# Kernel tuning notes

Measured on AMD Instinct MI355X. Metric: run time of the kernel, lower is better.

The kernel has to match this reference:

```python
import jax, jax.numpy as jnp
import numpy as np
import math

NUM_HEADS = 16
ROPE_BASE = 10000.0


def _rotate_half(x):
    d = x.shape[-1] // 2
    return jnp.concatenate([-x[..., d:], x[..., :d]], axis=-1)


def setup_inputs() -> dict:
    key = jax.random.key(0)
    ks = jax.random.split(key, 6)
    B, S, H = 2, 2048, 2048
    x = jax.random.normal(ks[0], (B, S, H), dtype=jnp.float32)
    # xavier_uniform for square [H,H]: limit = sqrt(6/(H+H))
    lim = math.sqrt(6.0 / (H + H))
    Wq = jax.random.uniform(ks[1], (H, H), minval=-lim, maxval=lim, dtype=jnp.float32)
    Wk = jax.random.uniform(ks[2], (H, H), minval=-lim, maxval=lim, dtype=jnp.float32)
    Wv = jax.random.uniform(ks[3], (H, H), minval=-lim, maxval=lim, dtype=jnp.float32)
    Wo = jax.random.uniform(ks[4], (H, H), minval=-lim, maxval=lim, dtype=jnp.float32)
    # bias_matrix initialized as tril(randn*0.02), matching _init_weights
    bias_matrix = jnp.tril(jax.random.normal(ks[5], (S, S), dtype=jnp.float32) * 0.02)
    return {"x": x, "Wq": Wq, "Wk": Wk, "Wv": Wv, "Wo": Wo, "bias_matrix": bias_matrix}


def reference(x, Wq, Wk, Wv, Wo, bias_matrix):
    B, S, hidden = x.shape
    H = NUM_HEADS
    D = hidden // H

    # projections (torch Linear: y = x @ W.T)
    def proj(W):
        return jnp.einsum('bsh,eh->bse', x, W).reshape(B, S, H, D).transpose(0, 2, 1, 3)

    q, k, v = proj(Wq), proj(Wk), proj(Wv)  # [B,H,S,D]

    # rotary embeddings
    inv_freq = 1.0 / (ROPE_BASE ** (jnp.arange(0, D, 2, dtype=jnp.float32) / D))
    t = jnp.arange(S, dtype=jnp.float32)
    freqs = t[:, None] * inv_freq[None, :]          # [S, D/2]
    emb = jnp.concatenate([freqs, freqs], axis=-1)  # [S, D]
    cos = jnp.cos(emb)[None, None]                  # [1,1,S,D]
    sin = jnp.sin(emb)[None, None]

    q = q * cos + _rotate_half(q) * sin
    k = k * cos + _rotate_half(k) * sin

    # contextual bias: bias_matrix[:S,:S], broadcast over batch & heads
    bias = bias_matrix[:S, :S][None, None]          # [1,1,S,S]
    bmean = jnp.mean(bias, axis=-1, keepdims=True) * 0.1  # [1,1,S,1]
    q = q + bmean
    k = k + bmean

    scores = jnp.einsum('bhqd,bhkd->bhqk', q, k) / math.sqrt(D)
    scores = scores + bias

    causal = jnp.triu(jnp.ones((S, S), dtype=bool), k=1)
    scores = jnp.where(causal[None, None], -jnp.inf, scores)

    attn_weights = jax.nn.softmax(scores, axis=-1)  # [B,H,S,S]
    attn_out = jnp.einsum('bhqk,bhkd->bhqd', attn_weights, v)
    attn_out = attn_out.transpose(0, 2, 1, 3).reshape(B, S, hidden)
    output = jnp.einsum('bsh,eh->bse', attn_out, Wo)
    return output, attn_weights
```

## Files before the change

### kernel.cpp

```cpp
#include <hip/hip_runtime.h>
#include <hip/hip_bf16.h>

typedef __bf16 bf16_t;
typedef __bf16 bf16x8 __attribute__((ext_vector_type(8)));
typedef float f32x4 __attribute__((ext_vector_type(4)));

#define SEQ 2048
#define HID 2048
#define NH 16
#define DH 128
#define BATCH 2

typedef __attribute__((address_space(1))) const unsigned int g_u32;
typedef __attribute__((address_space(3))) unsigned int l_u32;
#define GLOAD_LDS16(g, l) __builtin_amdgcn_global_load_lds((g_u32*)(g), (l_u32*)(l), 16, 0, 0)

__device__ __forceinline__ unsigned short f2bf(float f) {
  return __builtin_bit_cast(unsigned short, (__bf16)f);
}

__global__ void k_cast_bf16(const float4* __restrict__ in, ushort4* __restrict__ out, int n4) {
  int i = blockIdx.x * 256 + threadIdx.x;
  if (i >= n4) return;
  float4 v = in[i];
  ushort4 o;
  o.x = f2bf(v.x); o.y = f2bf(v.y); o.z = f2bf(v.z); o.w = f2bf(v.w);
  out[i] = o;
}

__global__ void k_bmean(const float* __restrict__ bias, float* __restrict__ bm) {
  int s = blockIdx.x;
  int t = threadIdx.x;
  const float4* row = (const float4*)(bias + (size_t)s * SEQ);
  float acc = 0.f;
  for (int c = t; c < SEQ / 4; c += 256) { float4 v = row[c]; acc += (v.x + v.y) + (v.z + v.w); }
  for (int off = 1; off < 64; off <<= 1) acc += __shfl_xor(acc, off);
  __shared__ float red[4];
  if ((t & 63) == 0) red[t >> 6] = acc;
  __syncthreads();
  if (t == 0) bm[s] = (red[0] + red[1] + red[2] + red[3]) * (0.1f / SEQ);
}

template <int EPI>
__global__ __launch_bounds__(256, 2) void k_gemm_bt(const bf16_t* __restrict__ A,
                                                    const bf16_t* __restrict__ B,
                                                    void* __restrict__ C,
                                                    int M, int N, int K) {
  __shared__ ushort As[128 * 64];
  __shared__ ushort Bs[128 * 64];
  const int tid = threadIdx.x;
  const int lane = tid & 63, wave = tid >> 6;
  const int m16 = lane & 15, quad = lane >> 4;
  const int wm = (wave >> 1) * 64, wn = (wave & 1) * 64;
  const int bm0 = blockIdx.y * 128, bn0 = blockIdx.x * 128;

  f32x4 acc[4][4];
  for (int i = 0; i < 4; ++i)
    for (int j = 0; j < 4; ++j) acc[i][j] = (f32x4){0.f, 0.f, 0.f, 0.f};

  const int NT = K / 64;
  for (int kt = 0; kt < NT; ++kt) {
    __syncthreads();
    size_t k0 = (size_t)kt * 64;
    for (int it = 0; it < 4; ++it) {
      int g = it * 256 + tid;
      int r = g >> 3;
      int c8 = (g & 7) ^ (r & 7);
      int base = (it * 256 + wave * 64) * 8;
      GLOAD_LDS16(A + (size_t)(bm0 + r) * K + k0 + c8 * 8, &As[base]);
      GLOAD_LDS16(B + (size_t)(bn0 + r) * K + k0 + c8 * 8, &Bs[base]);
    }
    __syncthreads();
    for (int ks = 0; ks < 2; ++ks) {
      bf16x8 af[4], bfr[4];
      for (int i = 0; i < 4; ++i) {
        int row = wm + i * 16 + m16;
        af[i] = *(const bf16x8*)&As[row * 64 + (((ks * 4 + quad) ^ (row & 7)) * 8)];
      }
      for (int j = 0; j < 4; ++j) {
        int row = wn + j * 16 + m16;
        bfr[j] = *(const bf16x8*)&Bs[row * 64 + (((ks * 4 + quad) ^ (row & 7)) * 8)];
      }
      for (int i = 0; i < 4; ++i)
        for (int j = 0; j < 4; ++j)
          acc[i][j] = __builtin_amdgcn_mfma_f32_16x16x32_bf16(af[i], bfr[j], acc[i][j], 0, 0, 0);
    }
  }
  for (int i = 0; i < 4; ++i)
    for (int j = 0; j < 4; ++j)
      for (int r = 0; r < 4; ++r) {
        int row = bm0 + wm + i * 16 + quad * 4 + r;
        int col = bn0 + wn + j * 16 + m16;
        float v = acc[i][j][r];
        if (EPI == 0) ((float*)C)[(size_t)row * N + col] = v;
        else          ((bf16_t*)C)[(size_t)row * N + col] = (bf16_t)v;
      }
}

__global__ __launch_bounds__(256, 2) void k_gemm_qkv(const bf16_t* __restrict__ A,
                                                     const bf16_t* __restrict__ B,
                                                     float* __restrict__ Qf,
                                                     float* __restrict__ Kf,
                                                     bf16_t* __restrict__ Vr) {
  __shared__ ushort As[128 * 64];
  __shared__ ushort Bs[128 * 64];
  const int tid = threadIdx.x;
  const int lane = tid & 63, wave = tid >> 6;
  const int m16 = lane & 15, quad = lane >> 4;
  const int wm = (wave >> 1) * 64, wn = (wave & 1) * 64;
  const int bm0 = blockIdx.y * 128, bn0 = blockIdx.x * 128;
  const int K = HID;

  f32x4 acc[4][4];
  for (int i = 0; i < 4; ++i)
    for (int j = 0; j < 4; ++j) acc[i][j] = (f32x4){0.f, 0.f, 0.f, 0.f};

  const int NT = K / 64;
  for (int kt = 0; kt < NT; ++kt) {
    __syncthreads();
    size_t k0 = (size_t)kt * 64;
    for (int it = 0; it < 4; ++it) {
      int g = it * 256 + tid;
      int r = g >> 3;
      int c8 = (g & 7) ^ (r & 7);
      int base = (it * 256 + wave * 64) * 8;
      GLOAD_LDS16(A + (size_t)(bm0 + r) * K + k0 + c8 * 8, &As[base]);
      GLOAD_LDS16(B + (size_t)(bn0 + r) * K + k0 + c8 * 8, &Bs[base]);
    }
    __syncthreads();
    for (int ks = 0; ks < 2; ++ks) {
      bf16x8 af[4], bfr[4];
      for (int i = 0; i < 4; ++i) {
        int row = wm + i * 16 + m16;
        af[i] = *(const bf16x8*)&As[row * 64 + (((ks * 4 + quad) ^ (row & 7)) * 8)];
      }
      for (int j = 0; j < 4; ++j) {
        int row = wn + j * 16 + m16;
        bfr[j] = *(const bf16x8*)&Bs[row * 64 + (((ks * 4 + quad) ^ (row & 7)) * 8)];
      }
      for (int i = 0; i < 4; ++i)
        for (int j = 0; j < 4; ++j)
          acc[i][j] = __builtin_amdgcn_mfma_f32_16x16x32_bf16(af[i], bfr[j], acc[i][j], 0, 0, 0);
    }
  }
  const int region = bn0 >> 11;
  for (int i = 0; i < 4; ++i)
    for (int j = 0; j < 4; ++j)
      for (int r = 0; r < 4; ++r) {
        int row = bm0 + wm + i * 16 + quad * 4 + r;
        int cl = (bn0 + wn + j * 16 + m16) & (HID - 1);
        float v = acc[i][j][r];
        if (region == 0)      Qf[(size_t)row * HID + cl] = v;
        else if (region == 1) Kf[(size_t)row * HID + cl] = v;
        else                  Vr[(size_t)row * HID + cl] = (bf16_t)v;
      }
}

__global__ void k_vtrans(const bf16_t* __restrict__ Vr, bf16_t* __restrict__ Vt) {
  __shared__ ushort T[64 * 72];
  const int tid = threadIdx.x;
  const int s0 = blockIdx.x * 64, c0 = blockIdx.y * 64, b = blockIdx.z;
  const int h = c0 >> 7, d0 = c0 & (DH - 1);
  int r = tid >> 2, cc = (tid & 3) * 16;
  const bf16_t* src = Vr + ((size_t)(b * SEQ + s0 + r)) * HID + c0 + cc;
  *(uint4*)&T[r * 72 + cc] = *(const uint4*)src;
  *(uint4*)&T[r * 72 + cc + 8] = *(const uint4*)(src + 8);
  __syncthreads();
  int dr = tid >> 2, sc0 = (tid & 3) * 16;
  ushort tmp[16];
  for (int e = 0; e < 16; ++e) tmp[e] = T[(sc0 + e) * 72 + dr];
  bf16_t* dst = Vt + ((size_t)(b * NH + h) * DH + d0 + dr) * SEQ + s0 + sc0;
  *(uint4*)dst = *(uint4*)&tmp[0];
  *(uint4*)(dst + 8) = *(uint4*)&tmp[8];
}

__global__ void k_rope(const float* __restrict__ Qf, const float* __restrict__ Kf,
                       const float* __restrict__ bm,
                       bf16_t* __restrict__ Qb, bf16_t* __restrict__ Kb) {
  int idx = blockIdx.x * 256 + threadIdx.x;
  int row = idx >> 8;
  int p = idx & 255;
  int h = p >> 4, i0 = (p & 15) * 4;
  int s = row & (SEQ - 1);
  float b = bm[s];
  size_t o1 = (size_t)row * HID + h * DH + i0;
  size_t o2 = o1 + 64;
  float4 q1 = *(const float4*)(Qf + o1);
  float4 q2 = *(const float4*)(Qf + o2);
  float4 k1 = *(const float4*)(Kf + o1);
  float4 k2 = *(const float4*)(Kf + o2);
  ushort4 q1o, q2o, k1o, k2o;
#pragma unroll
  for (int e = 0; e < 4; ++e) {
    float invf = exp2f((float)(i0 + e) * -0.2076205059304601f);
    float ang = (float)s * invf;
    float sn, cs;
    sincosf(ang, &sn, &cs);
    float q1e = (&q1.x)[e], q2e = (&q2.x)[e];
    float k1e = (&k1.x)[e], k2e = (&k2.x)[e];
    (&q1o.x)[e] = f2bf(q1e * cs - q2e * sn + b);
    (&q2o.x)[e] = f2bf(q2e * cs + q1e * sn + b);
    (&k1o.x)[e] = f2bf(k1e * cs - k2e * sn + b);
    (&k2o.x)[e] = f2bf(k2e * cs + k1e * sn + b);
  }
  *(ushort4*)(Qb + o1) = q1o;
  *(ushort4*)(Qb + o2) = q2o;
  *(ushort4*)(Kb + o1) = k1o;
  *(ushort4*)(Kb + o2) = k2o;
}

__global__ __launch_bounds__(256, 2) void k_attn(const bf16_t* __restrict__ Qb,
                                                 const bf16_t* __restrict__ Kb,
                                                 const bf16_t* __restrict__ Vt,
                                                 const bf16_t* __restrict__ Bb,
                                                 float* __restrict__ P,
                                                 bf16_t* __restrict__ AO) {
  __shared__ ushort Qs[64 * 128];
  __shared__ ushort Ks[2][64 * 128];
  __shared__ ushort Bs[2][64 * 64];
  __shared__ ushort Ps[64 * 72];

  const int tid = threadIdx.x;
  const int lane = tid & 63, wave = tid >> 6;
  const int m16 = lane & 15, quad = lane >> 4;
  const int h = blockIdx.y, b = blockIdx.z;
  const int wq = wave * 16;
  const float scale = 0.08838834764831845f;

  const bf16_t* Kbase = Kb + ((size_t)b * SEQ) * HID + (size_t)h * DH;
  const bf16_t* Vbase = Vt + ((size_t)(b * NH + h)) * DH * SEQ;

  auto stageK = [&](int kt, int buf) {
    const bf16_t* Kg = Kbase + (size_t)(kt * 64) * HID;
#pragma unroll
    for (int it = 0; it < 4; ++it) {
      int g = it * 256 + tid;
      int r = g >> 4;
      int c16 = (g & 15) ^ (r & 15);
      GLOAD_LDS16(Kg + (size_t)r * HID + c16 * 8, &Ks[buf][(it * 256 + wave * 64) * 8]);
    }
  };

  for (int half = 0; half < 2; ++half) {
    const int qt = half ? (int)blockIdx.x : 31 - (int)blockIdx.x;
    const int q0 = qt * 64;
    const bf16_t* Bgq = Bb + (size_t)q0 * SEQ;

    auto stageB = [&](int kt, int buf) {
      const bf16_t* Bg = Bgq + kt * 64;
#pragma unroll
      for (int it = 0; it < 2; ++it) {
        int g = it * 256 + tid;
        int r = g >> 3;
        int c8 = (g & 7) ^ (r & 7);
        GLOAD_LDS16(Bg + (size_t)r * SEQ + c8 * 8, &Bs[buf][(it * 256 + wave * 64) * 8]);
      }
    };

    __syncthreads();
    const bf16_t* Qg = Qb + ((size_t)(b * SEQ + q0)) * HID + (size_t)h * DH;
#pragma unroll
    for (int it = 0; it < 4; ++it) {
      int g = it * 256 + tid;
      int r = g >> 4;
      int c16 = (g & 15) ^ (r & 15);
      GLOAD_LDS16(Qg + (size_t)r * HID + c16 * 8, &Qs[(it * 256 + wave * 64) * 8]);
    }
    stageK(0, 0);
    stageB(0, 0);

    float m_ln[4], l_ln[4];
#pragma unroll
    for (int r = 0; r < 4; ++r) { m_ln[r] = -1e30f; l_ln[r] = 0.f; }

    for (int kt = 0; kt <= qt; ++kt) {
      const int cur = kt & 1;
      __syncthreads();
      if (kt < qt) { stageK(kt + 1, cur ^ 1); stageB(kt + 1, cur ^ 1); }

      f32x4 sc[4];
#pragma unroll
      for (int j = 0; j < 4; ++j) sc[j] = (f32x4){0.f, 0.f, 0.f, 0.f};
#pragma unroll
      for (int ks = 0; ks < 4; ++ks) {
        int qrow = wq + m16;
        bf16x8 af = *(const bf16x8*)&Qs[qrow * 128 + (((ks * 4 + quad) ^ (qrow & 15)) * 8)];
#pragma unroll
        for (int j = 0; j < 4; ++j) {
          int krow = j * 16 + m16;
          bf16x8 bfr = *(const bf16x8*)&Ks[cur][krow * 128 + (((ks * 4 + quad) ^ (krow & 15)) * 8)];
          sc[j] = __builtin_amdgcn_mfma_f32_16x16x32_bf16(af, bfr, sc[j], 0, 0, 0);
        }
      }
#pragma unroll
      for (int r = 0; r < 4; ++r) {
        int rl = wq + quad * 4 + r, qi = q0 + rl;
        float v[4], mx = m_ln[r];
#pragma unroll
        for (int j = 0; j < 4; ++j) {
          int c = j * 16 + m16;
          int ki = kt * 64 + c;
          float bv = (float)(*(const bf16_t*)&Bs[cur][rl * 64 + (((c >> 3) ^ (rl & 7)) << 3) + (c & 7)]);
          float xv = sc[j][r] * scale + bv;
          v[j] = (ki > qi) ? -1e30f : xv;
          mx = fmaxf(mx, v[j]);
        }
        float corr = __expf(m_ln[r] - mx);
        float s = __expf(v[0] - mx) + __expf(v[1] - mx) + __expf(v[2] - mx) + __expf(v[3] - mx);
        l_ln[r] = l_ln[r] * corr + s;
        m_ln[r] = mx;
      }
    }
    float mrow[4], linv[4];
#pragma unroll
    for (int r = 0; r < 4; ++r) {
      float m = m_ln[r], l = l_ln[r];
      for (int off = 1; off < 16; off <<= 1) {
        float mo = __shfl_xor(m, off), lo = __shfl_xor(l, off);
        float mn = fmaxf(m, mo);
        l = l * __expf(m - mn) + lo * __expf(mo - mn);
        m = mn;
      }
      mrow[r] = m; linv[r] = 1.f / l;
    }

    __syncthreads();
    stageK(0, 0);
    stageB(0, 0);

    f32x4 oacc[8];
#pragma unroll
    for (int d = 0; d < 8; ++d) oacc[d] = (f32x4){0.f, 0.f, 0.f, 0.f};
    float* Pg = P + (((size_t)(b * NH + h)) * SEQ + q0) * SEQ;

    for (int kt = 0; kt <= qt; ++kt) {
      const int cur = kt & 1;
      __syncthreads();
      if (kt < qt) { stageK(kt + 1, cur ^ 1); stageB(kt + 1, cur ^ 1); }

      f32x4 sc[4];
#pragma unroll
      for (int j = 0; j < 4; ++j) sc[j] = (f32x4){0.f, 0.f, 0.f, 0.f};
#pragma unroll
      for (int ks = 0; ks < 4; ++ks) {
        int qrow = wq + m16;
        bf16x8 af = *(const bf16x8*)&Qs[qrow * 128 + (((ks * 4 + quad) ^ (qrow & 15)) * 8)];
#pragma unroll
        for (int j = 0; j < 4; ++j) {
          int krow = j * 16 + m16;
          bf16x8 bfr = *(const bf16x8*)&Ks[cur][krow * 128 + (((ks * 4 + quad) ^ (krow & 15)) * 8)];
          sc[j] = __builtin_amdgcn_mfma_f32_16x16x32_bf16(af, bfr, sc[j], 0, 0, 0);
        }
      }

      bf16x8 vf0[8];
#pragma unroll
      for (int dt = 0; dt < 8; ++dt)
        vf0[dt] = *(const bf16x8*)(Vbase + (size_t)(dt * 16 + m16) * SEQ + kt * 64 + quad * 8);

#pragma unroll
      for (int r = 0; r < 4; ++r) {
        int rl = wq + quad * 4 + r, qi = q0 + rl;
#pragma unroll
        for (int j = 0; j < 4; ++j) {
          int c = j * 16 + m16;
          int ki = kt * 64 + c;
          float bv = (float)(*(const bf16_t*)&Bs[cur][rl * 64 + (((c >> 3) ^ (rl & 7)) << 3) + (c & 7)]);
          float xv = sc[j][r] * scale + bv;
          float p = (ki > qi) ? 0.f : __expf(xv - mrow[r]) * linv[r];
          Pg[(size_t)rl * SEQ + ki] = p;
          Ps[rl * 72 + j * 16 + m16] = f2bf(p);
        }
      }

      bf16x8 vf1[8];
#pragma unroll
      for (int dt = 0; dt < 8; ++dt)
        vf1[dt] = *(const bf16x8*)(Vbase + (size_t)(dt * 16 + m16) * SEQ + kt * 64 + 32 + quad * 8);

      {
        bf16x8 pf = *(const bf16x8*)&Ps[(wq + m16) * 72 + quad * 8];
#pragma unroll
        for (int dt = 0; dt < 8; ++dt)
          oacc[dt] = __builtin_amdgcn_mfma_f32_16x16x32_bf16(pf, vf0[dt], oacc[dt], 0, 0, 0);
        pf = *(const bf16x8*)&Ps[(wq + m16) * 72 + 32 + quad * 8];
#pragma unroll
        for (int dt = 0; dt < 8; ++dt)
          oacc[dt] = __builtin_amdgcn_mfma_f32_16x16x32_bf16(pf, vf1[dt], oacc[dt], 0, 0, 0);
      }
    }

    bf16_t* AOg = AO + ((size_t)(b * SEQ + q0)) * HID + (size_t)h * DH;
#pragma unroll
    for (int r = 0; r < 4; ++r) {
      int rl = wq + quad * 4 + r;
#pragma unroll
      for (int dt = 0; dt < 8; ++dt)
        AOg[(size_t)rl * HID + dt * 16 + m16] = (bf16_t)oacc[dt][r];
    }

    int kz0 = (qt + 1) * 64;
    for (int r = 0; r < 64; ++r) {
      float4* dst = (float4*)(Pg + (size_t)r * SEQ);
      for (int c = kz0 / 4 + tid; c < SEQ / 4; c += 256) dst[c] = make_float4(0.f, 0.f, 0.f, 0.f);
    }
  }
}

extern "C" void kernel_launch(void* const* d_in, const int* in_sizes, int n_in,
                              void* d_out, int out_size, void* d_ws, size_t ws_size,
                              hipStream_t stream) {
  const float* x = (const float*)d_in[0];
  const float* Wq = (const float*)d_in[1];
  const float* Wk = (const float*)d_in[2];
  const float* Wv = (const float*)d_in[3];
  const float* Wo = (const float*)d_in[4];
  const float* bias = (const float*)d_in[5];

  float* out = (float*)d_out;
  float* P = out + (size_t)BATCH * SEQ * HID;
  float* Qf = P;
  float* Kf = P + (size_t)BATCH * SEQ * HID;
  bf16_t* Vr = (bf16_t*)(P + 2 * (size_t)BATCH * SEQ * HID);

  char* w = (char*)d_ws;
  bf16_t* xb = (bf16_t*)w;  w += (size_t)BATCH * SEQ * HID * 2;
  bf16_t* Wqb = (bf16_t*)w; w += (size_t)HID * HID * 2;
  bf16_t* Wkb = (bf16_t*)w; w += (size_t)HID * HID * 2;
  bf16_t* Wvb = (bf16_t*)w; w += (size_t)HID * HID * 2;
  bf16_t* Wob = (bf16_t*)w; w += (size_t)HID * HID * 2;
  bf16_t* Qb = (bf16_t*)w;  w += (size_t)BATCH * SEQ * HID * 2;
  bf16_t* Kb = (bf16_t*)w;  w += (size_t)BATCH * SEQ * HID * 2;
  bf16_t* Vt = (bf16_t*)w;  w += (size_t)BATCH * SEQ * HID * 2;
  bf16_t* AO = (bf16_t*)w;  w += (size_t)BATCH * SEQ * HID * 2;
  float* bm = (float*)w;    w += (size_t)SEQ * 4;
  bf16_t* Bb = xb;

  const int n4x = BATCH * SEQ * HID / 4;
  const int n4w = HID * HID / 4;
  const int n4b = SEQ * SEQ / 4;
  k_cast_bf16<<<(n4x + 255) / 256, 256, 0, stream>>>((const float4*)x, (ushort4*)xb, n4x);
  k_cast_bf16<<<(n4w + 255) / 256, 256, 0, stream>>>((const float4*)Wq, (ushort4*)Wqb, n4w);
  k_cast_bf16<<<(n4w + 255) / 256, 256, 0, stream>>>((const float4*)Wk, (ushort4*)Wkb, n4w);
  k_cast_bf16<<<(n4w + 255) / 256, 256, 0, stream>>>((const float4*)Wv, (ushort4*)Wvb, n4w);
  k_cast_bf16<<<(n4w + 255) / 256, 256, 0, stream>>>((const float4*)Wo, (ushort4*)Wob, n4w);
  k_bmean<<<SEQ, 256, 0, stream>>>(bias, bm);

  k_gemm_qkv<<<dim3(3 * HID / 128, BATCH * SEQ / 128), 256, 0, stream>>>(xb, Wqb, Qf, Kf, Vr);

  k_cast_bf16<<<(n4b + 255) / 256, 256, 0, stream>>>((const float4*)bias, (ushort4*)Bb, n4b);

  k_vtrans<<<dim3(SEQ / 64, HID / 64, BATCH), 256, 0, stream>>>(Vr, Vt);
  k_rope<<<(BATCH * SEQ * HID / 8) / 256, 256, 0, stream>>>(Qf, Kf, bm, Qb, Kb);

  k_attn<<<dim3(16, NH, BATCH), 256, 0, stream>>>(Qb, Kb, Vt, Bb, P, AO);

  k_gemm_bt<0><<<dim3(HID / 128, BATCH * SEQ / 128), 256, 0, stream>>>(AO, Wob, out, BATCH * SEQ, HID, HID);
}
```

Measured before the change: 991.3 us.

## Keep Q fragments in registers, read bias directly, swizzle GEMM tile order

The attention kernel no longer stages Q and the bias tile in LDS. Each wave loads its Q MFMA fragments into registers once, and bias values come straight from global memory as scalar bf16 loads per kt tile. The freed LDS allows launch bounds to rise to 3 blocks per CU. Both GEMMs also remap block IDs with an XCD-style swizzle to improve L2 locality. The risks are uncoalesced 2-byte global bias loads with no prefetch overlap, and extra register pressure under the tighter occupancy bound.

```diff
diff --git a/kernel.cpp b/kernel.cpp
--- a/kernel.cpp
+++ b/kernel.cpp
@@ -52,7 +52,10 @@
   const int lane = tid & 63, wave = tid >> 6;
   const int m16 = lane & 15, quad = lane >> 4;
   const int wm = (wave >> 1) * 64, wn = (wave & 1) * 64;
-  const int bm0 = blockIdx.y * 128, bn0 = blockIdx.x * 128;
+  const int nwg = (int)(gridDim.x * gridDim.y);
+  int bid = (int)blockIdx.x + (int)gridDim.x * (int)blockIdx.y;
+  int swz = (bid & 7) * (nwg >> 3) + (bid >> 3);
+  const int bm0 = (swz / (int)gridDim.x) * 128, bn0 = (swz % (int)gridDim.x) * 128;
 
   f32x4 acc[4][4];
   for (int i = 0; i < 4; ++i)
@@ -108,7 +111,10 @@
   const int lane = tid & 63, wave = tid >> 6;
   const int m16 = lane & 15, quad = lane >> 4;
   const int wm = (wave >> 1) * 64, wn = (wave & 1) * 64;
-  const int bm0 = blockIdx.y * 128, bn0 = blockIdx.x * 128;
+  const int nwg = (int)(gridDim.x * gridDim.y);
+  int bid = (int)blockIdx.x + (int)gridDim.x * (int)blockIdx.y;
+  int swz = (bid & 7) * (nwg >> 3) + (bid >> 3);
+  const int bm0 = (swz / (int)gridDim.x) * 128, bn0 = (swz % (int)gridDim.x) * 128;
   const int K = HID;
 
   f32x4 acc[4][4];
@@ -209,15 +215,13 @@
   *(ushort4*)(Kb + o2) = k2o;
 }
 
-__global__ __launch_bounds__(256, 2) void k_attn(const bf16_t* __restrict__ Qb,
+__global__ __launch_bounds__(256, 3) void k_attn(const bf16_t* __restrict__ Qb,
                                                  const bf16_t* __restrict__ Kb,
                                                  const bf16_t* __restrict__ Vt,
                                                  const bf16_t* __restrict__ Bb,
                                                  float* __restrict__ P,
                                                  bf16_t* __restrict__ AO) {
-  __shared__ ushort Qs[64 * 128];
   __shared__ ushort Ks[2][64 * 128];
-  __shared__ ushort Bs[2][64 * 64];
   __shared__ ushort Ps[64 * 72];
 
   const int tid = threadIdx.x;
@@ -244,30 +248,16 @@
   for (int half = 0; half < 2; ++half) {
     const int qt = half ? (int)blockIdx.x : 31 - (int)blockIdx.x;
     const int q0 = qt * 64;
-    const bf16_t* Bgq = Bb + (size_t)q0 * SEQ;
-
-    auto stageB = [&](int kt, int buf) {
-      const bf16_t* Bg = Bgq + kt * 64;
-#pragma unroll
-      for (int it = 0; it < 2; ++it) {
-        int g = it * 256 + tid;
-        int r = g >> 3;
-        int c8 = (g & 7) ^ (r & 7);
-        GLOAD_LDS16(Bg + (size_t)r * SEQ + c8 * 8, &Bs[buf][(it * 256 + wave * 64) * 8]);
-      }
-    };
-
-    __syncthreads();
-    const bf16_t* Qg = Qb + ((size_t)(b * SEQ + q0)) * HID + (size_t)h * DH;
-#pragma unroll
-    for (int it = 0; it < 4; ++it) {
-      int g = it * 256 + tid;
-      int r = g >> 4;
-      int c16 = (g & 15) ^ (r & 15);
-      GLOAD_LDS16(Qg + (size_t)r * HID + c16 * 8, &Qs[(it * 256 + wave * 64) * 8]);
-    }
+
+    __syncthreads();
     stageK(0, 0);
-    stageB(0, 0);
+
+    const bf16_t* Qg = Qb + ((size_t)(b * SEQ + q0 + wq + m16)) * HID + (size_t)h * DH;
+    bf16x8 qf[4];
+#pragma unroll
+    for (int ks = 0; ks < 4; ++ks) qf[ks] = *(const bf16x8*)(Qg + ks * 32 + quad * 8);
+
+    const bf16_t* bl = Bb + (size_t)(q0 + wq + quad * 4) * SEQ + m16;
 
     float m_ln[4], l_ln[4];
 #pragma unroll
@@ -276,32 +266,35 @@
     for (int kt = 0; kt <= qt; ++kt) {
       const int cur = kt & 1;
       __syncthreads();
-      if (kt < qt) { stageK(kt + 1, cur ^ 1); stageB(kt + 1, cur ^ 1); }
+      if (kt < qt) stageK(kt + 1, cur ^ 1);
+
+      float bv[4][4];
+#pragma unroll
+      for (int r = 0; r < 4; ++r)
+#pragma unroll
+        for (int j = 0; j < 4; ++j)
+          bv[r][j] = (float)bl[(size_t)r * SEQ + kt * 64 + j * 16];
 
       f32x4 sc[4];
 #pragma unroll
       for (int j = 0; j < 4; ++j) sc[j] = (f32x4){0.f, 0.f, 0.f, 0.f};
 #pragma unroll
       for (int ks = 0; ks < 4; ++ks) {
-        int qrow = wq + m16;
-        bf16x8 af = *(const bf16x8*)&Qs[qrow * 128 + (((ks * 4 + quad) ^ (qrow & 15)) * 8)];
 #pragma unroll
         for (int j = 0; j < 4; ++j) {
           int krow = j * 16 + m16;
           bf16x8 bfr = *(const bf16x8*)&Ks[cur][krow * 128 + (((ks * 4 + quad) ^ (krow & 15)) * 8)];
-          sc[j] = __builtin_amdgcn_mfma_f32_16x16x32_bf16(af, bfr, sc[j], 0, 0, 0);
+          sc[j] = __builtin_amdgcn_mfma_f32_16x16x32_bf16(qf[ks], bfr, sc[j], 0, 0, 0);
         }
       }
 #pragma unroll
       for (int r = 0; r < 4; ++r) {
-        int rl = wq + quad * 4 + r, qi = q0 + rl;
+        int qi = q0 + wq + quad * 4 + r;
         float v[4], mx = m_ln[r];
 #pragma unroll
         for (int j = 0; j < 4; ++j) {
-          int c = j * 16 + m16;
-          int ki = kt * 64 + c;
-          float bv = (float)(*(const bf16_t*)&Bs[cur][rl * 64 + (((c >> 3) ^ (rl & 7)) << 3) + (c & 7)]);
-          float xv = sc[j][r] * scale + bv;
+          int ki = kt * 64 + j * 16 + m16;
+          float xv = sc[j][r] * scale + bv[r][j];
           v[j] = (ki > qi) ? -1e30f : xv;
           mx = fmaxf(mx, v[j]);
         }
@@ -326,7 +319,6 @@
 
     __syncthreads();
     stageK(0, 0);
-    stageB(0, 0);
 
     f32x4 oacc[8];
 #pragma unroll
@@ -336,20 +328,25 @@
     for (int kt = 0; kt <= qt; ++kt) {
       const int cur = kt & 1;
       __syncthreads();
-      if (kt < qt) { stageK(kt + 1, cur ^ 1); stageB(kt + 1, cur ^ 1); }
+      if (kt < qt) stageK(kt + 1, cur ^ 1);
+
+      float bv[4][4];
+#pragma unroll
+      for (int r = 0; r < 4; ++r)
+#pragma unroll
+        for (int j = 0; j < 4; ++j)
+          bv[r][j] = (float)bl[(size_t)r * SEQ + kt * 64 + j * 16];
 
       f32x4 sc[4];
 #pragma unroll
       for (int j = 0; j < 4; ++j) sc[j] = (f32x4){0.f, 0.f, 0.f, 0.f};
 #pragma unroll
       for (int ks = 0; ks < 4; ++ks) {
-        int qrow = wq + m16;
-        bf16x8 af = *(const bf16x8*)&Qs[qrow * 128 + (((ks * 4 + quad) ^ (qrow & 15)) * 8)];
 #pragma unroll
         for (int j = 0; j < 4; ++j) {
           int krow = j * 16 + m16;
           bf16x8 bfr = *(const bf16x8*)&Ks[cur][krow * 128 + (((ks * 4 + quad) ^ (krow & 15)) * 8)];
-          sc[j] = __builtin_amdgcn_mfma_f32_16x16x32_bf16(af, bfr, sc[j], 0, 0, 0);
+          sc[j] = __builtin_amdgcn_mfma_f32_16x16x32_bf16(qf[ks], bfr, sc[j], 0, 0, 0);
         }
       }
 
@@ -363,10 +360,8 @@
         int rl = wq + quad * 4 + r, qi = q0 + rl;
 #pragma unroll
         for (int j = 0; j < 4; ++j) {
-          int c = j * 16 + m16;
-          int ki = kt * 64 + c;
-          float bv = (float)(*(const bf16_t*)&Bs[cur][rl * 64 + (((c >> 3) ^ (rl & 7)) << 3) + (c & 7)]);
-          float xv = sc[j][r] * scale + bv;
+          int ki = kt * 64 + j * 16 + m16;
+          float xv = sc[j][r] * scale + bv[r][j];
           float p = (ki > qi) ? 0.f : __expf(xv - mrow[r]) * linv[r];
           Pg[(size_t)rl * SEQ + ki] = p;
           Ps[rl * 72 + j * 16 + m16] = f2bf(p);
```

Measured after the change: 1.161 ms. +17.2%, slower.
